# Optimization experiments

Hardware: AMD Instinct MI355X
Metric: run time of the kernel (lower is better)

Reference implementation:

```python
import jax, jax.numpy as jnp
import numpy as np

H, W = 512, 1024          # ERP panorama resolution
K = 15                    # neighbour_nb (degree_max)
N = H * W                 # pixel count (norm_const)
GAMMA = 0.1
MULTIPLIER = 1.0


def erp_dirs():
    """Unit ray directions for an equirectangular grid, shape [3, H, W].
    (EquirecGrid.to_xyz convention: pixel-centered lon/lat spherical rays.)"""
    lat = (0.5 - (jnp.arange(H, dtype=jnp.float32) + 0.5) / H) * jnp.pi       # [H]
    lon = ((jnp.arange(W, dtype=jnp.float32) + 0.5) / W - 0.5) * 2.0 * jnp.pi  # [W]
    lat = lat[:, None]
    lon = lon[None, :]
    x = jnp.cos(lat) * jnp.sin(lon)
    y = jnp.broadcast_to(jnp.sin(lat), (H, W))
    z = jnp.cos(lat) * jnp.cos(lon)
    return jnp.stack([x, y, z], axis=0)  # [3,H,W]


def setup_inputs() -> dict:
    key = jax.random.key(0)
    k1, k2, k3, k4 = jax.random.split(key, 4)
    sig1 = jax.random.uniform(k1, (1, 1, H, W), dtype=jnp.float32) * 10.0 + 0.1  # depth > 0
    sig2 = jax.random.normal(k2, (1, 3, H, W), dtype=jnp.float32)                # normals
    weights = jax.random.uniform(k3, (K, N), dtype=jnp.float32)                  # graph edge weights
    neighbours = jax.random.randint(k4, (K, N), 0, N, dtype=jnp.int64)           # neighbour pixel ids
    return {"sig1": sig1, "sig2": sig2, "weights": weights, "neighbours": neighbours}


def reference(sig1, sig2, weights, neighbours):
    dirs = erp_dirs()                       # [3,H,W]
    p = (sig1[0, 0] * dirs).reshape(3, -1)  # cam points, [3,N]
    n = sig2[0].reshape(3, -1)              # normals,    [3,N]

    pn = jnp.sum(p * n, axis=0)             # <p_i, n_i>, [N]
    p_nb = p[:, neighbours]                 # gathered neighbour points,  [3,K,N]
    n_nb = n[:, neighbours]                 # gathered neighbour normals, [3,K,N]

    # aux1[k,i] = <p_i, n_i> - <p_{nb(k,i)}, n_i>
    aux1 = pn[None, :] - jnp.sum(p_nb * n[:, None, :], axis=0)   # [K,N]
    # aux2[k,i] = || n_i - n_{nb(k,i)} ||_2
    aux2 = jnp.linalg.norm(n[:, None, :] - n_nb, axis=0)         # [K,N]

    term1 = jnp.linalg.norm(aux1 * weights, axis=0).sum()        # norm over K, sum over pixels
    term2 = (aux2 * weights).sum()
    loss = (term1 + GAMMA * term2) / N
    return MULTIPLIER * loss
```

## Files before the change

### kernel.cpp

```cpp
#include <hip/hip_runtime.h>
#include <math.h>

#define HH 512
#define WW 1024
#define NPIX (HH * WW)
#define KK 15
#define GAMMA 0.1f
#define MULTIPLIER 1.0f


__global__ __launch_bounds__(256) void prep_kernel(
    const float* __restrict__ sig1,
    const float* __restrict__ sig2,
    float4* __restrict__ pk,
    float* __restrict__ acc) {
  int i = blockIdx.x * 256 + threadIdx.x;
  if (i == 0) acc[0] = 0.0f;
  if (i >= NPIX) return;

  int h = i >> 10;
  int w = i & (WW - 1);
  const float PI = 3.14159265358979323846f;
  float lat = (0.5f - (h + 0.5f) * (1.0f / HH)) * PI;
  float lon = ((w + 0.5f) * (1.0f / WW) - 0.5f) * (2.0f * PI);
  float sla, cla, slo, clo;
  sincosf(lat, &sla, &cla);
  sincosf(lon, &slo, &clo);
  float dx = cla * slo;
  float dy = sla;
  float dz = cla * clo;

  float s = sig1[i];
  float nx = sig2[i];
  float ny = sig2[NPIX + i];
  float nz = sig2[2 * NPIX + i];

  float px = s * dx, py = s * dy, pz = s * dz;
  float pn = px * nx + py * ny + pz * nz;

  pk[2 * i + 0] = make_float4(px, py, pz, pn);
  pk[2 * i + 1] = make_float4(nx, ny, nz, 0.0f);
}

__global__ __launch_bounds__(256) void main_kernel(
    const float4* __restrict__ pk,
    const float* __restrict__ weights,
    const int* __restrict__ nb,
    float* __restrict__ acc) {
  int i = blockIdx.x * 256 + threadIdx.x;
  float local = 0.0f;

  if (i < NPIX) {
    float4 a = pk[2 * i + 0];
    float4 b = pk[2 * i + 1];
    float pn = a.w;
    float nx = b.x, ny = b.y, nz = b.z;

    float sq = 0.0f, t2 = 0.0f;
#pragma unroll
    for (int k = 0; k < KK; ++k) {
      int j = nb[k * NPIX + i];
      float wgt = weights[k * NPIX + i];
      float4 pj = pk[2 * j + 0];
      float4 nj = pk[2 * j + 1];
      float aux1 = pn - (pj.x * nx + pj.y * ny + pj.z * nz);
      float ddx = nx - nj.x, ddy = ny - nj.y, ddz = nz - nj.z;
      float aux2 = sqrtf(ddx * ddx + ddy * ddy + ddz * ddz);
      float aw = aux1 * wgt;
      sq += aw * aw;
      t2 += aux2 * wgt;
    }
    local = sqrtf(sq) + GAMMA * t2;
  }

  for (int off = 32; off > 0; off >>= 1)
    local += __shfl_down(local, off, 64);

  __shared__ float smem[4];
  int lane = threadIdx.x & 63;
  int wid = threadIdx.x >> 6;
  if (lane == 0) smem[wid] = local;
  __syncthreads();
  if (threadIdx.x == 0) {
    float s = smem[0] + smem[1] + smem[2] + smem[3];
    atomicAdd(acc, s);
  }
}

__global__ void fin_kernel(const float* __restrict__ acc, float* __restrict__ out) {
  if (threadIdx.x == 0 && blockIdx.x == 0)
    out[0] = MULTIPLIER * acc[0] * (1.0f / (float)NPIX);
}

extern "C" void kernel_launch(void* const* d_in, const int* in_sizes, int n_in,
                              void* d_out, int out_size, void* d_ws, size_t ws_size,
                              hipStream_t stream) {
  const float* sig1 = (const float*)d_in[0];
  const float* sig2 = (const float*)d_in[1];
  const float* wts  = (const float*)d_in[2];
  const int*   nb   = (const int*)d_in[3];
  float* out = (float*)d_out;

  float*  acc = (float*)d_ws;
  float4* pk  = (float4*)((char*)d_ws + 256);

  int blocks = NPIX / 256;
  hipLaunchKernelGGL(prep_kernel, dim3(blocks), dim3(256), 0, stream, sig1, sig2, pk, acc);
  hipLaunchKernelGGL(main_kernel, dim3(blocks), dim3(256), 0, stream, pk, wts, nb, acc);
  hipLaunchKernelGGL(fin_kernel, dim3(1), dim3(64), 0, stream, acc, out);
}
```

Baseline: 216.8 us.

## Pack points and normals into 16-byte half-precision records and batch gathers

Per-pixel points and normals are now stored as fp16 pairs in a single uint4, with <p,n> kept in fp32. This halves the record size, so each random neighbour gather touches one 16-byte record instead of two float4s. The main kernel also issues all neighbour-index loads, then all gathers, then all weight loads before computing, which exposes more memory-level parallelism at the cost of more registers. Prep switches to fast __sinf/__cosf, and the bounds checks are removed. This adds fp16 rounding error on the geometry terms.

```diff
diff --git a/kernel.cpp b/kernel.cpp
--- a/kernel.cpp
+++ b/kernel.cpp
@@ -1,4 +1,5 @@
 #include <hip/hip_runtime.h>
+#include <hip/hip_fp16.h>
 #include <math.h>
 
 #define HH 512
@@ -9,23 +10,30 @@
 #define MULTIPLIER 1.0f
 
 
+__device__ inline unsigned int pack2f(float a, float b) {
+  __half2 h = __floats2half2_rn(a, b);
+  return *(unsigned int*)&h;
+}
+__device__ inline float2 up2(unsigned int u) {
+  __half2 h = *(__half2*)&u;
+  return __half22float2(h);
+}
+
 __global__ __launch_bounds__(256) void prep_kernel(
     const float* __restrict__ sig1,
     const float* __restrict__ sig2,
-    float4* __restrict__ pk,
+    uint4* __restrict__ pack,
     float* __restrict__ acc) {
   int i = blockIdx.x * 256 + threadIdx.x;
   if (i == 0) acc[0] = 0.0f;
-  if (i >= NPIX) return;
 
   int h = i >> 10;
   int w = i & (WW - 1);
   const float PI = 3.14159265358979323846f;
   float lat = (0.5f - (h + 0.5f) * (1.0f / HH)) * PI;
   float lon = ((w + 0.5f) * (1.0f / WW) - 0.5f) * (2.0f * PI);
-  float sla, cla, slo, clo;
-  sincosf(lat, &sla, &cla);
-  sincosf(lon, &slo, &clo);
+  float sla = __sinf(lat), cla = __cosf(lat);
+  float slo = __sinf(lon), clo = __cosf(lon);
   float dx = cla * slo;
   float dy = sla;
   float dz = cla * clo;
@@ -38,40 +46,52 @@
   float px = s * dx, py = s * dy, pz = s * dz;
   float pn = px * nx + py * ny + pz * nz;
 
-  pk[2 * i + 0] = make_float4(px, py, pz, pn);
-  pk[2 * i + 1] = make_float4(nx, ny, nz, 0.0f);
+  uint4 u;
+  u.x = pack2f(px, py);
+  u.y = pack2f(pz, nx);
+  u.z = pack2f(ny, nz);
+  u.w = __float_as_uint(pn);
+  pack[i] = u;
 }
 
 __global__ __launch_bounds__(256) void main_kernel(
-    const float4* __restrict__ pk,
+    const uint4* __restrict__ pack,
     const float* __restrict__ weights,
     const int* __restrict__ nb,
     float* __restrict__ acc) {
   int i = blockIdx.x * 256 + threadIdx.x;
-  float local = 0.0f;
 
-  if (i < NPIX) {
-    float4 a = pk[2 * i + 0];
-    float4 b = pk[2 * i + 1];
-    float pn = a.w;
-    float nx = b.x, ny = b.y, nz = b.z;
+  int j[KK];
+#pragma unroll
+  for (int k = 0; k < KK; ++k) j[k] = nb[k * NPIX + i];
 
-    float sq = 0.0f, t2 = 0.0f;
+  uint4 g[KK];
 #pragma unroll
-    for (int k = 0; k < KK; ++k) {
-      int j = nb[k * NPIX + i];
-      float wgt = weights[k * NPIX + i];
-      float4 pj = pk[2 * j + 0];
-      float4 nj = pk[2 * j + 1];
-      float aux1 = pn - (pj.x * nx + pj.y * ny + pj.z * nz);
-      float ddx = nx - nj.x, ddy = ny - nj.y, ddz = nz - nj.z;
-      float aux2 = sqrtf(ddx * ddx + ddy * ddy + ddz * ddz);
-      float aw = aux1 * wgt;
-      sq += aw * aw;
-      t2 += aux2 * wgt;
-    }
-    local = sqrtf(sq) + GAMMA * t2;
+  for (int k = 0; k < KK; ++k) g[k] = pack[j[k]];
+
+  float wv[KK];
+#pragma unroll
+  for (int k = 0; k < KK; ++k) wv[k] = weights[k * NPIX + i];
+
+  uint4 c = pack[i];
+  float2 cy = up2(c.y), cz = up2(c.z);
+  float nix = cy.y, niy = cz.x, niz = cz.y;
+  float pn = __uint_as_float(c.w);
+
+  float sq = 0.0f, t2 = 0.0f;
+#pragma unroll
+  for (int k = 0; k < KK; ++k) {
+    float2 gx = up2(g[k].x);
+    float2 gy = up2(g[k].y);
+    float2 gz = up2(g[k].z);
+    float aux1 = pn - (gx.x * nix + gx.y * niy + gy.x * niz);
+    float ddx = nix - gy.y, ddy = niy - gz.x, ddz = niz - gz.y;
+    float aux2 = sqrtf(ddx * ddx + ddy * ddy + ddz * ddz);
+    float aw = aux1 * wv[k];
+    sq += aw * aw;
+    t2 += aux2 * wv[k];
   }
+  float local = sqrtf(sq) + GAMMA * t2;
 
   for (int off = 32; off > 0; off >>= 1)
     local += __shfl_down(local, off, 64);
@@ -101,11 +121,11 @@
   const int*   nb   = (const int*)d_in[3];
   float* out = (float*)d_out;
 
-  float*  acc = (float*)d_ws;
-  float4* pk  = (float4*)((char*)d_ws + 256);
+  float* acc = (float*)d_ws;
+  uint4* pack = (uint4*)((char*)d_ws + 256);
 
   int blocks = NPIX / 256;
-  hipLaunchKernelGGL(prep_kernel, dim3(blocks), dim3(256), 0, stream, sig1, sig2, pk, acc);
-  hipLaunchKernelGGL(main_kernel, dim3(blocks), dim3(256), 0, stream, pk, wts, nb, acc);
+  hipLaunchKernelGGL(prep_kernel, dim3(blocks), dim3(256), 0, stream, sig1, sig2, pack, acc);
+  hipLaunchKernelGGL(main_kernel, dim3(blocks), dim3(256), 0, stream, pack, wts, nb, acc);
   hipLaunchKernelGGL(fin_kernel, dim3(1), dim3(64), 0, stream, acc, out);
 }
```

New measurement: 174.5 us. 19.5% less time.
